# Performance work log

Measured on AMD Instinct MI355X. Metric: run time of the kernel, lower is better.

## Reference

```python
import jax, jax.numpy as jnp
import numpy as np

D_MODEL = 1024
D_STATE = 16
D_CONV = 4
EXPAND = 2
D_INNER = EXPAND * D_MODEL  # 2048
BATCH = 2
SEQ = 2048


def setup_inputs() -> dict:
    key = jax.random.key(0)
    ks = jax.random.split(key, 7)
    s = 0.02
    x = jax.random.normal(ks[0], (BATCH, SEQ, D_MODEL), jnp.float32)
    in_proj_w = jax.random.normal(ks[1], (2 * D_INNER, D_MODEL), jnp.float32) * s
    conv_w = jax.random.normal(ks[2], (D_INNER, 1, D_CONV), jnp.float32) * s  # depthwise: groups=d_inner
    conv_b = jnp.zeros((D_INNER,), jnp.float32)
    x_proj_w = jax.random.normal(ks[3], (2 * D_STATE, D_INNER), jnp.float32) * s
    dt_proj_w = jax.random.normal(ks[4], (D_INNER, D_INNER), jnp.float32) * s
    dt_proj_b = jnp.zeros((D_INNER,), jnp.float32)
    # A = arange(1..d_state) repeated for each inner channel; A_log = log(A)
    A_log = jnp.log(jnp.tile(jnp.arange(1, D_STATE + 1, dtype=jnp.float32), (D_INNER, 1)))
    D_param = jnp.ones((D_INNER,), jnp.float32)
    out_proj_w = jax.random.normal(ks[5], (D_MODEL, D_INNER), jnp.float32) * s
    return {"x": x, "in_proj_w": in_proj_w, "conv_w": conv_w, "conv_b": conv_b,
            "x_proj_w": x_proj_w, "dt_proj_w": dt_proj_w, "dt_proj_b": dt_proj_b,
            "A_log": A_log, "D_param": D_param, "out_proj_w": out_proj_w}


def reference(x, in_proj_w, conv_w, conv_b, x_proj_w, dt_proj_w, dt_proj_b, A_log, D_param, out_proj_w):
    B, L, _ = x.shape
    # input projection -> [B, L, 2*d_inner], split into ssm path and gate
    xz = x @ in_proj_w.T
    x_ssm, z = jnp.split(xz, 2, axis=-1)

    # causal depthwise conv1d (torch pads both sides by d_conv-1 then slices [:L])
    xc = jnp.transpose(x_ssm, (0, 2, 1))  # [B, d_inner, L]
    xc = jnp.pad(xc, ((0, 0), (0, 0), (D_CONV - 1, 0)))
    xc = jax.lax.conv_general_dilated(
        xc, conv_w, window_strides=(1,), padding='VALID',
        dimension_numbers=('NCH', 'OIH', 'NCH'), feature_group_count=D_INNER)
    xc = xc + conv_b[None, :, None]
    x_act = jax.nn.silu(jnp.transpose(xc, (0, 2, 1)))  # [B, L, d_inner]

    delta = jax.nn.softplus(x_act @ dt_proj_w.T + dt_proj_b)  # [B, L, d_inner]
    bc = x_act @ x_proj_w.T                                   # [B, L, 2*d_state]
    B_p, C_p = jnp.split(bc, 2, axis=-1)

    A = -jnp.exp(A_log)  # [d_inner, d_state]

    def step(h, inp):
        u_i, d_i, B_i, C_i = inp  # [B,d], [B,d], [B,n], [B,n]
        dA = jnp.exp(d_i[..., None] * A)                       # [B, d, n]
        h = dA * h + (d_i * u_i)[..., None] * B_i[:, None, :]  # [B, d, n]
        y = jnp.einsum('bdn,bn->bd', h, C_i)
        return h, y

    h0 = jnp.zeros((B, D_INNER, D_STATE), x.dtype)
    seq = (jnp.swapaxes(x_act, 0, 1), jnp.swapaxes(delta, 0, 1),
           jnp.swapaxes(B_p, 0, 1), jnp.swapaxes(C_p, 0, 1))
    _, ys = jax.lax.scan(step, h0, seq)  # ys: [L, B, d_inner]
    y_ssm = jnp.swapaxes(ys, 0, 1) + x_act * D_param

    y = y_ssm * jax.nn.silu(z)
    return y @ out_proj_w.T
```

## Files before the change

kernel.cpp:

```cpp
#include <hip/hip_runtime.h>
#include <hip/hip_bf16.h>
#include <math.h>

#define DM 1024
#define DS 16
#define DI 2048
#define NB 2
#define LL 2048
#define BL (NB*LL)
#define LC 32
#define NC (LL/LC)

typedef __attribute__((ext_vector_type(8))) short short8;
typedef __attribute__((ext_vector_type(8))) unsigned short ushort8;
typedef __attribute__((ext_vector_type(4))) float f32x4;

__device__ __forceinline__ float silu_f(float x){ return x / (1.f + __expf(-x)); }
__device__ __forceinline__ float softplus_f(float x){ return (x > 15.f) ? x : log1pf(__expf(x)); }
__device__ __forceinline__ unsigned short f2bf(float f){
  unsigned u = __float_as_uint(f);
  u += 0x7fff + ((u >> 16) & 1);
  return (unsigned short)(u >> 16);
}
__device__ __forceinline__ float bf2f(unsigned short v){
  return __uint_as_float(((unsigned)v) << 16);
}

__global__ __launch_bounds__(256) void f2b_k(const float* __restrict__ src,
                                             unsigned short* __restrict__ dst, int n)
{
  int i = (blockIdx.x * 256 + threadIdx.x) * 8;
  if (i >= n) return;
  float4 v0 = *(const float4*)&src[i];
  float4 v1 = *(const float4*)&src[i + 4];
  ushort8 o;
  o[0]=f2bf(v0.x); o[1]=f2bf(v0.y); o[2]=f2bf(v0.z); o[3]=f2bf(v0.w);
  o[4]=f2bf(v1.x); o[5]=f2bf(v1.y); o[6]=f2bf(v1.z); o[7]=f2bf(v1.w);
  *(ushort8*)&dst[i] = o;
}

__global__ __launch_bounds__(256) void f2b_multi(
    const float* __restrict__ s0, unsigned short* __restrict__ d0, int c0,
    const float* __restrict__ s1, unsigned short* __restrict__ d1, int c1,
    const float* __restrict__ s2, unsigned short* __restrict__ d2, int c2,
    const float* __restrict__ s3, unsigned short* __restrict__ d3, int c3)
{
  int b = blockIdx.x;
  const float* s; unsigned short* d;
  if (b < c0)              { s = s0; d = d0; }
  else if ((b -= c0) < c1) { s = s1; d = d1; }
  else if ((b -= c1) < c2) { s = s2; d = d2; }
  else                     { b -= c2; s = s3; d = d3; }
  int i = (b * 256 + threadIdx.x) * 8;
  float4 v0 = *(const float4*)&s[i];
  float4 v1 = *(const float4*)&s[i + 4];
  ushort8 o;
  o[0]=f2bf(v0.x); o[1]=f2bf(v0.y); o[2]=f2bf(v0.z); o[3]=f2bf(v0.w);
  o[4]=f2bf(v1.x); o[5]=f2bf(v1.y); o[6]=f2bf(v1.z); o[7]=f2bf(v1.w);
  *(ushort8*)&d[i] = o;
}

template<int EPI, int OUTBF>
__global__ __launch_bounds__(256) void gemm7(
    const unsigned short* __restrict__ A, const unsigned short* __restrict__ Bw,
    const float* __restrict__ bias, void* __restrict__ Cp,
    int N, int K)
{
  __shared__ unsigned short lds[256 * 64];
  const int t = threadIdx.x;
  const int wid = t >> 6, lane = t & 63;
  const int nbx = N >> 7;
  const int cpx = (int)gridDim.x >> 3;
  const int bid = (int)blockIdx.x;
  const int swz = (bid & 7) * cpx + (bid >> 3);
  const int bm = (swz / nbx) << 7, bn = (swz % nbx) << 7;
  const int wm = (wid >> 1) * 64, wn = (wid & 1) * 64;
  const int ln15 = lane & 15, l16 = lane >> 4, lx7 = lane & 7;
  const int srow = lane >> 3;
  const int sch  = lx7 ^ srow;

  f32x4 acc[4][4] = {};

  for (int kt = 0; kt < (K >> 6); kt++) {
    const int k0 = kt << 6;
    __syncthreads();
    #pragma unroll
    for (int s = 0; s < 8; s++) {
      int g = wid * 8 + s;
      int row = g * 8 + srow;
      const unsigned short* src;
      if (g < 16) src = A  + (size_t)(bm + row) * K + k0 + sch * 8;
      else        src = Bw + (size_t)(bn + row - 128) * K + k0 + sch * 8;
      __builtin_amdgcn_global_load_lds(
          (const __attribute__((address_space(1))) void*)src,
          (__attribute__((address_space(3))) void*)(&lds[g * 512]), 16, 0, 0);
    }
    __syncthreads();
    short8 af[2][4], bfr[2][4];
    #pragma unroll
    for (int ks = 0; ks < 2; ks++) {
      int cc = ((ks << 2) + l16) ^ lx7;
      #pragma unroll
      for (int i = 0; i < 4; i++) {
        af[ks][i]  = *(const short8*)&lds[(wm + i * 16 + ln15) * 64 + cc * 8];
        bfr[ks][i] = *(const short8*)&lds[(128 + wn + i * 16 + ln15) * 64 + cc * 8];
      }
    }
    #pragma unroll
    for (int ks = 0; ks < 2; ks++)
      #pragma unroll
      for (int i = 0; i < 4; i++)
        #pragma unroll
        for (int j = 0; j < 4; j++)
          acc[i][j] = __builtin_amdgcn_mfma_f32_16x16x32_bf16(af[ks][i], bfr[ks][j], acc[i][j], 0, 0, 0);
  }

  #pragma unroll
  for (int i = 0; i < 4; i++) {
    #pragma unroll
    for (int j = 0; j < 4; j++) {
      int col = bn + wn + j * 16 + ln15;
      float bv = (EPI == 1) ? bias[col] : 0.f;
      #pragma unroll
      for (int r = 0; r < 4; r++) {
        int row = bm + wm + i * 16 + l16 * 4 + r;
        float v = acc[i][j][r];
        if (EPI == 1) v = softplus_f(v + bv);
        if (OUTBF) ((unsigned short*)Cp)[(size_t)row * N + col] = f2bf(v);
        else       ((float*)Cp)[(size_t)row * N + col] = v;
      }
    }
  }
}

__global__ __launch_bounds__(256) void conv_silu_k(
    const unsigned short* __restrict__ xz, const float* __restrict__ cw,
    const float* __restrict__ cb, unsigned short* __restrict__ xa)
{
  int v = blockIdx.x * 256 + threadIdx.x;
  int d8 = (v & (DI/8 - 1)) * 8;
  int bl = v >> 8;
  int l  = bl & (LL - 1);
  float acc[8];
  #pragma unroll
  for (int j = 0; j < 8; j++) acc[j] = cb[d8 + j];
  size_t rowb = (size_t)bl * (2 * DI) + d8;
  #pragma unroll
  for (int k = 0; k < 4; k++) {
    int ls = l - 3 + k;
    if (ls >= 0) {
      ushort8 xv = *(const ushort8*)&xz[rowb + (size_t)(k - 3) * (2 * DI)];
      #pragma unroll
      for (int j = 0; j < 8; j++) acc[j] += bf2f(xv[j]) * cw[(d8 + j) * 4 + k];
    }
  }
  ushort8 o;
  #pragma unroll
  for (int j = 0; j < 8; j++) o[j] = f2bf(silu_f(acc[j]));
  *(ushort8*)&xa[(size_t)bl * DI + d8] = o;
}

__global__ __launch_bounds__(256) void bc_k(
    const unsigned short* __restrict__ xa, const unsigned short* __restrict__ w,
    float* __restrict__ bc)
{
  __shared__ unsigned short sx[8 * DI];
  const int t = threadIdx.x;
  const size_t base = (size_t)blockIdx.x * 8 * DI;
  #pragma unroll
  for (int it = 0; it < 8; it++) {
    int v = t + it * 256;
    *(ushort8*)&sx[v * 8] = *(const ushort8*)&xa[base + (size_t)v * 8];
  }
  __syncthreads();
  const int m = t >> 5, n = t & 31;
  const unsigned short* wr = w + (size_t)n * DI;
  const unsigned short* xr = sx + m * DI;
  float acc = 0.f;
  #pragma unroll 4
  for (int k = 0; k < DI; k += 8) {
    ushort8 xv = *(const ushort8*)&xr[k];
    ushort8 wv = *(const ushort8*)&wr[k];
    #pragma unroll
    for (int j = 0; j < 8; j++) acc += bf2f(xv[j]) * bf2f(wv[j]);
  }
  bc[(size_t)(blockIdx.x * 8 + m) * 32 + n] = acc;
}

__global__ __launch_bounds__(256) void scan_part1(
    const float* __restrict__ dlt, const unsigned short* __restrict__ xa,
    const float* __restrict__ bc, const float* __restrict__ A_log,
    float* __restrict__ S_arr, float* __restrict__ sumdlt)
{
  const int bid = blockIdx.x;
  const int b = bid >> 9;
  const int c = (bid >> 3) & (NC - 1);
  const int dg = bid & 7;
  const int t = threadIdx.x;
  const int d = dg * 256 + t;
  float Ac[16];
  #pragma unroll
  for (int n = 0; n < 16; n++) Ac[n] = -__expf(A_log[d * 16 + n]);
  __shared__ float sB[LC][16];
  for (int e = t; e < LC * 16; e += 256) {
    int l = e >> 4, n = e & 15;
    sB[l][n] = bc[(size_t)(b * LL + c * LC + l) * 32 + n];
  }
  __syncthreads();
  float h[16] = {};
  float sd = 0.f;
  size_t rowbase = (size_t)(b * LL + c * LC) * DI + d;
  for (int l = 0; l < LC; l++) {
    float dl = dlt[rowbase + (size_t)l * DI];
    float u  = bf2f(xa[rowbase + (size_t)l * DI]);
    float w = dl * u;
    sd += dl;
    #pragma unroll
    for (int n = 0; n < 16; n++) {
      float dA = __expf(dl * Ac[n]);
      h[n] = dA * h[n] + w * sB[l][n];
    }
  }
  float* Sp = S_arr + ((size_t)(b * NC + c) * DI + d) * 16;
  #pragma unroll
  for (int n = 0; n < 16; n++) Sp[n] = h[n];
  sumdlt[(size_t)(b * NC + c) * DI + d] = sd;
}

__global__ __launch_bounds__(256) void scan_combine(
    const float* __restrict__ A_log, const float* __restrict__ sumdlt,
    float* __restrict__ S_arr)
{
  int tid = blockIdx.x * 256 + threadIdx.x;
  int n = tid & 15;
  int d = (tid >> 4) & (DI - 1);
  int b = tid >> 15;
  float Ac = -__expf(A_log[d * 16 + n]);
  float h = 0.f;
  for (int c = 0; c < NC; c++) {
    size_t idx = ((size_t)(b * NC + c) * DI + d) * 16 + n;
    float S = S_arr[idx];
    float P = __expf(sumdlt[(size_t)(b * NC + c) * DI + d] * Ac);
    S_arr[idx] = h;
    h = P * h + S;
  }
}

__global__ __launch_bounds__(256) void scan_part2(
    const float* __restrict__ dlt, const unsigned short* __restrict__ xa,
    const float* __restrict__ bc, const float* __restrict__ A_log,
    const float* __restrict__ Dp, const unsigned short* __restrict__ xz,
    const float* __restrict__ Hin, unsigned short* __restrict__ y)
{
  const int bid = blockIdx.x;
  const int b = bid >> 9;
  const int c = (bid >> 3) & (NC - 1);
  const int dg = bid & 7;
  const int t = threadIdx.x;
  const int d = dg * 256 + t;
  float Ac[16];
  #pragma unroll
  for (int n = 0; n < 16; n++) Ac[n] = -__expf(A_log[d * 16 + n]);
  __shared__ float sB[LC][16];
  __shared__ float sC[LC][16];
  for (int e = t; e < LC * 16; e += 256) {
    int l = e >> 4, n = e & 15;
    size_t row = (size_t)(b * LL + c * LC + l) * 32;
    sB[l][n] = bc[row + n];
    sC[l][n] = bc[row + 16 + n];
  }
  __syncthreads();
  float h[16];
  const float* Hp = Hin + ((size_t)(b * NC + c) * DI + d) * 16;
  #pragma unroll
  for (int n = 0; n < 16; n++) h[n] = Hp[n];
  const float Dv = Dp[d];
  size_t rowbase = (size_t)(b * LL + c * LC) * DI + d;
  for (int l = 0; l < LC; l++) {
    float dl = dlt[rowbase + (size_t)l * DI];
    float u  = bf2f(xa[rowbase + (size_t)l * DI]);
    float w = dl * u;
    float ya = 0.f;
    #pragma unroll
    for (int n = 0; n < 16; n++) {
      float dA = __expf(dl * Ac[n]);
      h[n] = dA * h[n] + w * sB[l][n];
      ya += h[n] * sC[l][n];
    }
    float zz = bf2f(xz[(size_t)(b * LL + c * LC + l) * (2 * DI) + DI + d]);
    y[rowbase + (size_t)l * DI] = f2bf((ya + u * Dv) * silu_f(zz));
  }
}

extern "C" void kernel_launch(void* const* d_in, const int* in_sizes, int n_in,
                              void* d_out, int out_size, void* d_ws, size_t ws_size,
                              hipStream_t stream)
{
  const float* x    = (const float*)d_in[0];
  const float* Win  = (const float*)d_in[1];
  const float* cw   = (const float*)d_in[2];
  const float* cb   = (const float*)d_in[3];
  const float* Wxp  = (const float*)d_in[4];
  const float* Wdt  = (const float*)d_in[5];
  const float* bdt  = (const float*)d_in[6];
  const float* Alog = (const float*)d_in[7];
  const float* Dp   = (const float*)d_in[8];
  const float* Wout = (const float*)d_in[9];
  float* out = (float*)d_out;

  float* ws = (float*)d_ws;
  float* dlt    = ws;
  float* bcb    = dlt + 8388608;
  float* S_arr  = bcb + 131072;
  float* sumdlt = S_arr + 4194304;
  unsigned short* xz_bf = (unsigned short*)(sumdlt + 262144);
  unsigned short* xa_bf = xz_bf + 16777216;
  unsigned short* y_bf  = xa_bf + 8388608;
  unsigned short* x_bf  = y_bf;
  unsigned short* win_bf= y_bf + 4194304;
  unsigned short* wbuf  = y_bf + 8388608;
  unsigned short* wxp_bf= wbuf + 4194304;

  f2b_multi<<<dim3(2048 + 2048 + 2048 + 32), dim3(256), 0, stream>>>(
      x, x_bf, 2048, Win, win_bf, 2048, Wdt, wbuf, 2048, Wxp, wxp_bf, 32);
  gemm7<0,1><<<dim3(1024), dim3(256), 0, stream>>>(x_bf, win_bf, nullptr, xz_bf, 2*DI, DM);
  conv_silu_k<<<dim3(BL*DI/8/256), dim3(256), 0, stream>>>(xz_bf, cw, cb, xa_bf);
  gemm7<1,0><<<dim3(512), dim3(256), 0, stream>>>(xa_bf, wbuf, bdt, dlt, DI, DI);
  f2b_k<<<dim3(DM*DI/2048), dim3(256), 0, stream>>>(Wout, wbuf, DM*DI);
  bc_k<<<dim3(BL/8), dim3(256), 0, stream>>>(xa_bf, wxp_bf, bcb);
  scan_part1<<<dim3(NB*NC*8), dim3(256), 0, stream>>>(dlt, xa_bf, bcb, Alog, S_arr, sumdlt);
  scan_combine<<<dim3(NB*DI*DS/256), dim3(256), 0, stream>>>(Alog, sumdlt, S_arr);
  scan_part2<<<dim3(NB*NC*8), dim3(256), 0, stream>>>(dlt, xa_bf, bcb, Alog, Dp, xz_bf, S_arr, y_bf);
  gemm7<0,0><<<dim3(256), dim3(256), 0, stream>>>(y_bf, wbuf, nullptr, out, DM, DI);
}
```

Before: 382.0 us.

## Enlarge GEMM tiles to 256x128 and store delta as bf16

Grows the GEMM block tile from 128x128 to 256x128, so each wave computes 128x64 with an 8x4 MFMA accumulator array. This raises operand reuse per LDS load and halves the grid size. The dt_proj GEMM output (delta) is now written as bf16 instead of fp32, which halves its write and its later reads in both scan passes at some precision cost. The larger accumulator raises register pressure, and the smaller grids (128 blocks for out_proj) may leave compute units idle.

New measurement: 395.9 us. +3.6%, slower.

```diff
diff --git a/kernel.cpp b/kernel.cpp
--- a/kernel.cpp
+++ b/kernel.cpp
@@ -61,62 +61,61 @@
 }
 
 template<int EPI, int OUTBF>
-__global__ __launch_bounds__(256) void gemm7(
+__global__ __launch_bounds__(256, 2) void gemm8(
     const unsigned short* __restrict__ A, const unsigned short* __restrict__ Bw,
     const float* __restrict__ bias, void* __restrict__ Cp,
     int N, int K)
 {
-  __shared__ unsigned short lds[256 * 64];
+  __shared__ unsigned short lds[384 * 64];
   const int t = threadIdx.x;
   const int wid = t >> 6, lane = t & 63;
   const int nbx = N >> 7;
   const int cpx = (int)gridDim.x >> 3;
   const int bid = (int)blockIdx.x;
   const int swz = (bid & 7) * cpx + (bid >> 3);
-  const int bm = (swz / nbx) << 7, bn = (swz % nbx) << 7;
-  const int wm = (wid >> 1) * 64, wn = (wid & 1) * 64;
+  const int bm = (swz / nbx) << 8, bn = (swz % nbx) << 7;
+  const int wm = (wid >> 1) * 128, wn = (wid & 1) * 64;
   const int ln15 = lane & 15, l16 = lane >> 4, lx7 = lane & 7;
   const int srow = lane >> 3;
   const int sch  = lx7 ^ srow;
 
-  f32x4 acc[4][4] = {};
+  f32x4 acc[8][4] = {};
 
   for (int kt = 0; kt < (K >> 6); kt++) {
     const int k0 = kt << 6;
     __syncthreads();
     #pragma unroll
-    for (int s = 0; s < 8; s++) {
-      int g = wid * 8 + s;
+    for (int s = 0; s < 12; s++) {
+      int g = wid * 12 + s;
       int row = g * 8 + srow;
       const unsigned short* src;
-      if (g < 16) src = A  + (size_t)(bm + row) * K + k0 + sch * 8;
-      else        src = Bw + (size_t)(bn + row - 128) * K + k0 + sch * 8;
+      if (g < 32) src = A  + (size_t)(bm + row) * K + k0 + sch * 8;
+      else        src = Bw + (size_t)(bn + row - 256) * K + k0 + sch * 8;
       __builtin_amdgcn_global_load_lds(
           (const __attribute__((address_space(1))) void*)src,
           (__attribute__((address_space(3))) void*)(&lds[g * 512]), 16, 0, 0);
     }
     __syncthreads();
-    short8 af[2][4], bfr[2][4];
     #pragma unroll
     for (int ks = 0; ks < 2; ks++) {
-      int cc = ((ks << 2) + l16) ^ lx7;
-      #pragma unroll
-      for (int i = 0; i < 4; i++) {
-        af[ks][i]  = *(const short8*)&lds[(wm + i * 16 + ln15) * 64 + cc * 8];
-        bfr[ks][i] = *(const short8*)&lds[(128 + wn + i * 16 + ln15) * 64 + cc * 8];
-      }
-    }
-    #pragma unroll
-    for (int ks = 0; ks < 2; ks++)
-      #pragma unroll
-      for (int i = 0; i < 4; i++)
+      const int cc = ((ks << 2) + l16) ^ lx7;
+      short8 af[8], bfr[4];
+      #pragma unroll
+      for (int i = 0; i < 8; i++)
+        af[i] = *(const short8*)&lds[(wm + i * 16 + ln15) * 64 + cc * 8];
+      #pragma unroll
+      for (int j = 0; j < 4; j++)
+        bfr[j] = *(const short8*)&lds[(256 + wn + j * 16 + ln15) * 64 + cc * 8];
+      #pragma unroll
+      for (int i = 0; i < 8; i++)
         #pragma unroll
         for (int j = 0; j < 4; j++)
-          acc[i][j] = __builtin_amdgcn_mfma_f32_16x16x32_bf16(af[ks][i], bfr[ks][j], acc[i][j], 0, 0, 0);
-  }
-
-  #pragma unroll
-  for (int i = 0; i < 4; i++) {
+          acc[i][j] = __builtin_amdgcn_mfma_f32_16x16x32_bf16(af[i], bfr[j], acc[i][j], 0, 0, 0);
+    }
+  }
+
+  #pragma unroll
+  for (int i = 0; i < 8; i++) {
     #pragma unroll
     for (int j = 0; j < 4; j++) {
       int col = bn + wn + j * 16 + ln15;
@@ -188,7 +187,7 @@
 }
 
 __global__ __launch_bounds__(256) void scan_part1(
-    const float* __restrict__ dlt, const unsigned short* __restrict__ xa,
+    const unsigned short* __restrict__ dlt, const unsigned short* __restrict__ xa,
     const float* __restrict__ bc, const float* __restrict__ A_log,
     float* __restrict__ S_arr, float* __restrict__ sumdlt)
 {
@@ -211,7 +210,7 @@
   float sd = 0.f;
   size_t rowbase = (size_t)(b * LL + c * LC) * DI + d;
   for (int l = 0; l < LC; l++) {
-    float dl = dlt[rowbase + (size_t)l * DI];
+    float dl = bf2f(dlt[rowbase + (size_t)l * DI]);
     float u  = bf2f(xa[rowbase + (size_t)l * DI]);
     float w = dl * u;
     sd += dl;
@@ -247,7 +246,7 @@
 }
 
 __global__ __launch_bounds__(256) void scan_part2(
-    const float* __restrict__ dlt, const unsigned short* __restrict__ xa,
+    const unsigned short* __restrict__ dlt, const unsigned short* __restrict__ xa,
     const float* __restrict__ bc, const float* __restrict__ A_log,
     const float* __restrict__ Dp, const unsigned short* __restrict__ xz,
     const float* __restrict__ Hin, unsigned short* __restrict__ y)
@@ -277,7 +276,7 @@
   const float Dv = Dp[d];
   size_t rowbase = (size_t)(b * LL + c * LC) * DI + d;
   for (int l = 0; l < LC; l++) {
-    float dl = dlt[rowbase + (size_t)l * DI];
+    float dl = bf2f(dlt[rowbase + (size_t)l * DI]);
     float u  = bf2f(xa[rowbase + (size_t)l * DI]);
     float w = dl * u;
     float ya = 0.f;
@@ -309,8 +308,8 @@
   float* out = (float*)d_out;
 
   float* ws = (float*)d_ws;
-  float* dlt    = ws;
-  float* bcb    = dlt + 8388608;
+  unsigned short* dlt_bf = (unsigned short*)ws;
+  float* bcb    = ws + 8388608;
   float* S_arr  = bcb + 131072;
   float* sumdlt = S_arr + 4194304;
   unsigned short* xz_bf = (unsigned short*)(sumdlt + 262144);
@@ -323,13 +322,13 @@
 
   f2b_multi<<<dim3(2048 + 2048 + 2048 + 32), dim3(256), 0, stream>>>(
       x, x_bf, 2048, Win, win_bf, 2048, Wdt, wbuf, 2048, Wxp, wxp_bf, 32);
-  gemm7<0,1><<<dim3(1024), dim3(256), 0, stream>>>(x_bf, win_bf, nullptr, xz_bf, 2*DI, DM);
+  gemm8<0,1><<<dim3(512), dim3(256), 0, stream>>>(x_bf, win_bf, nullptr, xz_bf, 2*DI, DM);
   conv_silu_k<<<dim3(BL*DI/8/256), dim3(256), 0, stream>>>(xz_bf, cw, cb, xa_bf);
-  gemm7<1,0><<<dim3(512), dim3(256), 0, stream>>>(xa_bf, wbuf, bdt, dlt, DI, DI);
+  gemm8<1,1><<<dim3(256), dim3(256), 0, stream>>>(xa_bf, wbuf, bdt, dlt_bf, DI, DI);
   f2b_k<<<dim3(DM*DI/2048), dim3(256), 0, stream>>>(Wout, wbuf, DM*DI);
   bc_k<<<dim3(BL/8), dim3(256), 0, stream>>>(xa_bf, wxp_bf, bcb);
-  scan_part1<<<dim3(NB*NC*8), dim3(256), 0, stream>>>(dlt, xa_bf, bcb, Alog, S_arr, sumdlt);
+  scan_part1<<<dim3(NB*NC*8), dim3(256), 0, stream>>>(dlt_bf, xa_bf, bcb, Alog, S_arr, sumdlt);
   scan_combine<<<dim3(NB*DI*DS/256), dim3(256), 0, stream>>>(Alog, sumdlt, S_arr);
-  scan_part2<<<dim3(NB*NC*8), dim3(256), 0, stream>>>(dlt, xa_bf, bcb, Alog, Dp, xz_bf, S_arr, y_bf);
-  gemm7<0,0><<<dim3(256), dim3(256), 0, stream>>>(y_bf, wbuf, nullptr, out, DM, DI);
-}
+  scan_part2<<<dim3(NB*NC*8), dim3(256), 0, stream>>>(dlt_bf, xa_bf, bcb, Alog, Dp, xz_bf, S_arr, y_bf);
+  gemm8<0,0><<<dim3(128), dim3(256), 0, stream>>>(y_bf, wbuf, nullptr, out, DM, DI);
+}
```
